# Kernel tuning notes

Measured on AMD Instinct MI355X. Metric: run time of the kernel, lower is better.

Reference implementation:

```python
import jax, jax.numpy as jnp
import numpy as np

DIM = 1024
NUM_ATT = 8
NUM_HEADS = 16
HEAD_DIM = DIM // NUM_HEADS
ROPE_BASE = 10000.0
NEG_INF = -1e9


def _rope(x):
    # x: [B, H, L, hd]; torchtune-style interleaved RoPE applied along the sequence axis.
    B, H, L, hd = x.shape
    pos = jnp.arange(L, dtype=jnp.float32)
    inv_freq = 1.0 / (ROPE_BASE ** (jnp.arange(0, hd, 2, dtype=jnp.float32) / hd))
    ang = pos[:, None] * inv_freq[None, :]          # [L, hd/2]
    cos = jnp.cos(ang)[None, None]                  # [1,1,L,hd/2]
    sin = jnp.sin(ang)[None, None]
    xr = x.reshape(B, H, L, hd // 2, 2)
    x0, x1 = xr[..., 0], xr[..., 1]
    out = jnp.stack([x0 * cos - x1 * sin, x1 * cos + x0 * sin], axis=-1)
    return out.reshape(B, H, L, hd).astype(x.dtype)


def setup_inputs() -> dict:
    key = jax.random.key(0)
    ks = jax.random.split(key, 7)
    B, L = 32, 512
    x = jax.random.normal(ks[0], (B, L, DIM), dtype=jnp.float32)
    s = 0.02  # init scale for numerical sanity (init choice, not math)
    query_projs = jax.random.normal(ks[1], (NUM_ATT, DIM, DIM), dtype=jnp.float32) * s
    key_projs = jax.random.normal(ks[2], (NUM_ATT, DIM, DIM), dtype=jnp.float32) * s
    value_projs = jax.random.normal(ks[3], (NUM_ATT, DIM, DIM), dtype=jnp.float32) * s
    out_projs = jax.random.normal(ks[4], (NUM_ATT, DIM, DIM), dtype=jnp.float32) * s
    router_w = jax.random.normal(ks[5], (DIM, NUM_ATT), dtype=jnp.float32) * s
    router_b = jnp.zeros((NUM_ATT,), dtype=jnp.float32)
    return {"x": x, "query_projs": query_projs, "key_projs": key_projs,
            "value_projs": value_projs, "out_projs": out_projs,
            "router_w": router_w, "router_b": router_b}


def reference(x, query_projs, key_projs, value_projs, out_projs, router_w, router_b):
    B, L, D = x.shape
    H, hd = NUM_HEADS, HEAD_DIM
    scale = hd ** -0.5

    # top-1 routing on mean-pooled tokens
    logits = x.mean(axis=1) @ router_w + router_b       # [B, E]
    attn_probs = jax.nn.softmax(logits, axis=-1)
    routes = jnp.argmax(attn_probs, axis=-1)            # [B] int

    # per-batch weight gather (the memory-bound irregular access) + bmm
    qw = query_projs[routes]                             # [B, D, D]
    kw = key_projs[routes]
    vw = value_projs[routes]
    q = jnp.einsum('bld,bde->ble', x, qw)
    k = jnp.einsum('bld,bde->ble', x, kw)
    v = jnp.einsum('bld,bde->ble', x, vw)

    q = q.reshape(B, L, H, hd).transpose(0, 2, 1, 3)     # [B,H,L,hd]
    k = k.reshape(B, L, H, hd).transpose(0, 2, 1, 3)
    v = v.reshape(B, L, H, hd).transpose(0, 2, 1, 3)

    q = _rope(q)
    k = _rope(k)

    scores = jnp.einsum('bhld,bhmd->bhlm', q, k) * scale  # [B,H,L,L]
    causal = jnp.triu(jnp.ones((L, L), dtype=bool), k=1)  # True above diag = masked
    scores = jnp.where(causal[None, None], NEG_INF, scores)
    attn = jax.nn.softmax(scores, axis=-1)
    out = jnp.einsum('bhlm,bhmd->bhld', attn, v)          # [B,H,L,hd]
    out = out.transpose(0, 2, 1, 3).reshape(B, L, D)

    ow = out_projs[routes]                                # [B, D, D]
    out = jnp.einsum('bld,bde->ble', out, ow)
    return out, attn_probs
```

## Files before the change

kernel.cpp:

```cpp
#include <hip/hip_runtime.h>


typedef __attribute__((ext_vector_type(8))) short bf16x8;
typedef __attribute__((ext_vector_type(4))) float f32x4;

typedef const __attribute__((address_space(1))) unsigned short* gas_t;
typedef __attribute__((address_space(3))) unsigned short* las_t;

#define OFF_PART   (0ull)
#define OFF_ROUTES (2ull << 20)
#define OFF_XB     (3ull << 20)
#define OFF_WT     (40ull << 20)
#define OFF_QKV    (112ull << 20)

__device__ __forceinline__ unsigned short f2bf(float f){
  unsigned int u = __float_as_uint(f);
  u += 0x7fffu + ((u >> 16) & 1u);
  return (unsigned short)(u >> 16);
}


__global__ void meanpool_kernel(const float* __restrict__ x, float* __restrict__ part,
                                unsigned short* __restrict__ xb){
  const int b = blockIdx.x, lc = blockIdx.y, t = threadIdx.x;
  const size_t base = ((size_t)b*512 + lc*32)*1024;
  const float* xs = x + base;
  unsigned short* xo = xb + base;
  float a0=0.f, a1=0.f, a2=0.f, a3=0.f;
  for (int l = 0; l < 32; ++l){
    const float* row = xs + l*1024;
    unsigned short* orow = xo + l*1024;
    const float v0 = row[t], v1 = row[t+256], v2 = row[t+512], v3 = row[t+768];
    a0 += v0; a1 += v1; a2 += v2; a3 += v3;
    orow[t] = f2bf(v0); orow[t+256] = f2bf(v1); orow[t+512] = f2bf(v2); orow[t+768] = f2bf(v3);
  }
  float* o = part + ((size_t)b*16 + lc)*1024;
  o[t] = a0; o[t+256] = a1; o[t+512] = a2; o[t+768] = a3;
}

__global__ void router_kernel(const float* __restrict__ part,
                              const float* __restrict__ rw,
                              const float* __restrict__ rbias,
                              float* __restrict__ probs,
                              int* __restrict__ routes){
  const int b = blockIdx.x, t = threadIdx.x;
  __shared__ float xbar[1024];
  __shared__ float red[256*8];
  #pragma unroll
  for (int k = 0; k < 4; ++k){
    const int d = t + k*256;
    float s = 0.f;
    for (int lc = 0; lc < 16; ++lc) s += part[((size_t)b*16 + lc)*1024 + d];
    xbar[d] = s * (1.0f/512.0f);
  }
  __syncthreads();
  float p[8] = {0.f,0.f,0.f,0.f,0.f,0.f,0.f,0.f};
  #pragma unroll
  for (int k = 0; k < 4; ++k){
    const int d = t + k*256;
    const float xv = xbar[d];
    #pragma unroll
    for (int e = 0; e < 8; ++e) p[e] = fmaf(xv, rw[d*8 + e], p[e]);
  }
  #pragma unroll
  for (int e = 0; e < 8; ++e) red[t*8 + e] = p[e];
  __syncthreads();
  for (int s2 = 128; s2 > 0; s2 >>= 1){
    if (t < s2){
      #pragma unroll
      for (int e = 0; e < 8; ++e) red[t*8 + e] += red[(t + s2)*8 + e];
    }
    __syncthreads();
  }
  if (t == 0){
    float lg[8], mx = -3e38f; int am = 0;
    #pragma unroll
    for (int e = 0; e < 8; ++e){
      lg[e] = red[e] + rbias[e];
      if (lg[e] > mx){ mx = lg[e]; am = e; }
    }
    float sum = 0.f, ex[8];
    #pragma unroll
    for (int e = 0; e < 8; ++e){ ex[e] = __expf(lg[e] - mx); sum += ex[e]; }
    const float inv = 1.0f / sum;
    #pragma unroll
    for (int e = 0; e < 8; ++e) probs[b*8 + e] = ex[e] * inv;
    routes[b] = am;
  }
}


__global__ void wcast_kernel(const float* __restrict__ W, unsigned short* __restrict__ Wt){
  __shared__ float tile[32][33];
  const int mtx = blockIdx.z;
  const float* Wm = W + (size_t)mtx*1024*1024;
  unsigned short* Wo = Wt + (size_t)mtx*1024*1024;
  const int t = threadIdx.x;
  const int c = t & 31, r0 = t >> 5;
  const int gx = blockIdx.x*32, gy = blockIdx.y*32;
  #pragma unroll
  for (int k = 0; k < 4; ++k){
    const int r = r0 + k*8;
    tile[r][c] = Wm[(size_t)(gy + r)*1024 + gx + c];
  }
  __syncthreads();
  #pragma unroll
  for (int k = 0; k < 4; ++k){
    const int r = r0 + k*8;
    Wo[(size_t)(gx + r)*1024 + gy + c] = f2bf(tile[c][r]);
  }
}


template<int MODE>
__global__ __launch_bounds__(256, 2) void gemm_kernel(
    const unsigned short* __restrict__ A,
    const unsigned short* __restrict__ Wt,
    const int* __restrict__ routes,
    unsigned short* __restrict__ qkvout,
    float* __restrict__ outf)
{
  __shared__ __align__(16) unsigned short As[3][128*32];
  __shared__ __align__(16) unsigned short Bs[3][128*32];

  int wg = blockIdx.x + (blockIdx.y << 3) + (blockIdx.z << 5);
  wg = (wg & 7) * ((MODE == 0) ? 384 : 128) + (wg >> 3);
  const int z   = wg >> 5;
  const int rem = wg & 31;
  const int m0  = (rem >> 3) * 128;
  const int n0  = (rem & 7) * 128;
  const int b = (MODE == 0) ? (z / 3) : z;
  const int p = (MODE == 0) ? (z - b*3) : 0;

  const int route = routes[b];
  const unsigned short* Ab = A + (size_t)b*512*1024;
  const unsigned short* Wb = Wt + (size_t)((MODE == 0) ? (p*8 + route) : route)*1024*1024;
  const int t = threadIdx.x;
  const int lane = t & 63;
  const int wave = t >> 6;
  const int wm = (wave >> 1) * 64;
  const int wn = (wave & 1) * 64;
  const int quad = lane >> 4;
  const int ln = lane & 15;

  f32x4 acc[4][4] = {};

  const int u0 = t, u1 = t + 256;
  const int r0s = u0 >> 2, c0s = (u0 & 3) ^ ((r0s >> 1) & 3);
  const int r1s = u1 >> 2, c1s = (u1 & 3) ^ ((r1s >> 1) & 3);
  const unsigned short* gA0 = Ab + (size_t)(m0 + r0s)*1024 + c0s*8;
  const unsigned short* gA1 = Ab + (size_t)(m0 + r1s)*1024 + c1s*8;
  const unsigned short* gB0 = Wb + (size_t)(n0 + r0s)*1024 + c0s*8;
  const unsigned short* gB1 = Wb + (size_t)(n0 + r1s)*1024 + c1s*8;
  las_t lA0 = (las_t)(&As[0][0] + u0*8), lA1 = (las_t)(&As[0][0] + u1*8);
  las_t lB0 = (las_t)(&Bs[0][0] + u0*8), lB1 = (las_t)(&Bs[0][0] + u1*8);

  const int swz = (quad ^ ((ln >> 1) & 3)) * 8;
  int offA[4], offB[4];
  #pragma unroll
  for (int i = 0; i < 4; ++i){
    offA[i] = (wm + i*16 + ln)*32 + swz;
    offB[i] = (wn + i*16 + ln)*32 + swz;
  }

#define STAGE(buf, kk) do { \
    const int bo_ = (buf)*4096; \
    __builtin_amdgcn_global_load_lds((gas_t)(gA0 + (kk)), lA0 + bo_, 16, 0, 0); \
    __builtin_amdgcn_global_load_lds((gas_t)(gA1 + (kk)), lA1 + bo_, 16, 0, 0); \
    __builtin_amdgcn_global_load_lds((gas_t)(gB0 + (kk)), lB0 + bo_, 16, 0, 0); \
    __builtin_amdgcn_global_load_lds((gas_t)(gB1 + (kk)), lB1 + bo_, 16, 0, 0); \
  } while (0)

#define COMPUTE(buf) do { \
    const unsigned short* Al_ = &As[buf][0]; \
    const unsigned short* Bl_ = &Bs[buf][0]; \
    bf16x8 av[4], bv[4]; \
    _Pragma("unroll") \
    for (int i = 0; i < 4; ++i){ \
      av[i] = *(const bf16x8*)(Al_ + offA[i]); \
      bv[i] = *(const bf16x8*)(Bl_ + offB[i]); \
    } \
    __builtin_amdgcn_s_setprio(1); \
    _Pragma("unroll") \
    for (int i = 0; i < 4; ++i) \
      _Pragma("unroll") \
      for (int j = 0; j < 4; ++j) \
        acc[i][j] = __builtin_amdgcn_mfma_f32_16x16x32_bf16(av[i], bv[j], acc[i][j], 0, 0, 0); \
    __builtin_amdgcn_s_setprio(0); \
  } while (0)

  STAGE(0, 0);
  STAGE(1, 32);
  for (int t8 = 0; t8 < 30; ++t8){
    asm volatile("s_waitcnt vmcnt(4)" ::: "memory");
    __builtin_amdgcn_s_barrier();
    __builtin_amdgcn_sched_barrier(0);
    STAGE((t8 + 2) % 3, t8*32 + 64);
    COMPUTE(t8 % 3);
  }
  asm volatile("s_waitcnt vmcnt(4)" ::: "memory");
  __builtin_amdgcn_s_barrier();
  __builtin_amdgcn_sched_barrier(0);
  COMPUTE(0);
  asm volatile("s_waitcnt vmcnt(0)" ::: "memory");
  __builtin_amdgcn_s_barrier();
  __builtin_amdgcn_sched_barrier(0);
  COMPUTE(1);
#undef STAGE
#undef COMPUTE

  if (MODE == 0){
    const size_t PSZ = (size_t)32*16*512*64;
    if (p < 2){
      #pragma unroll
      for (int j = 0; j < 4; ++j){
        const int e  = n0 + wn + j*16 + ln;
        const int h  = e >> 6;
        const int eh = e & 63;
        const float invf = exp2f(-0.41524101f * (float)(eh >> 1));
        float s1, c1; __sincosf(invf, &s1, &c1);
        unsigned short* outp = qkvout + ((((size_t)p*32 + b)*16 + h)*512)*64 + eh;
        const int l0 = m0 + wm + quad*4;
        #pragma unroll
        for (int i = 0; i < 4; ++i){
          float sn, cs;
          __sincosf((float)(l0 + i*16) * invf, &sn, &cs);
          #pragma unroll
          for (int r = 0; r < 4; ++r){
            const int l = l0 + i*16 + r;
            const float own = acc[i][j][r];
            const float par = __shfl_xor(own, 1, 64);
            const float v = (e & 1) ? fmaf(own, cs, par*sn) : fmaf(own, cs, -par*sn);
            outp[(size_t)l*64] = f2bf(v);
            const float nc = cs*c1 - sn*s1;
            const float ns = sn*c1 + cs*s1;
            cs = nc; sn = ns;
          }
        }
      }
    } else {
      #pragma unroll
      for (int j = 0; j < 4; ++j){
        const int e  = n0 + wn + j*16 + ln;
        const int h  = e >> 6;
        const int eh = e & 63;
        unsigned short* outp = qkvout + 2*PSZ + (((size_t)b*16 + h)*64 + eh)*512;
        #pragma unroll
        for (int i = 0; i < 4; ++i){
          const int l0 = m0 + wm + i*16 + quad*4;
          ushort4 pk;
          pk.x = f2bf(acc[i][j][0]); pk.y = f2bf(acc[i][j][1]);
          pk.z = f2bf(acc[i][j][2]); pk.w = f2bf(acc[i][j][3]);
          *(ushort4*)(outp + l0) = pk;
        }
      }
    }
  } else {
    #pragma unroll
    for (int j = 0; j < 4; ++j){
      const int e = n0 + wn + j*16 + ln;
      #pragma unroll
      for (int i = 0; i < 4; ++i){
        #pragma unroll
        for (int r = 0; r < 4; ++r){
          const int l = m0 + wm + i*16 + quad*4 + r;
          outf[((size_t)b*512 + l)*1024 + e] = acc[i][j][r];
        }
      }
    }
  }
}


#define PSTR 72

__global__ __launch_bounds__(256, 3) void attn_kernel(
    const unsigned short* __restrict__ qkv,
    unsigned short* __restrict__ ctx)
{
  __shared__ __align__(16) unsigned short Ks[2][64*64];
  __shared__ __align__(16) unsigned short Vts[2][64*64];
  __shared__ __align__(16) unsigned short Ps[4][32*PSTR];

  int wg = blockIdx.x + (blockIdx.y << 2) + (blockIdx.z << 6);
  wg = (wg & 7) * 256 + (wg >> 3);
  const int b  = wg >> 6;
  const int h  = (wg >> 2) & 15;
  const int qt = wg & 3;

  const size_t HO  = (((size_t)b)*16 + h)*512*64;
  const size_t PSZ = (size_t)32*16*512*64;
  const unsigned short* Qg  = qkv + HO;
  const unsigned short* Kg  = qkv + PSZ + HO;
  const unsigned short* Vtg = qkv + 2*PSZ + HO;

  const int t    = threadIdx.x;
  const int lane = t & 63;
  const int wave = t >> 6;
  const int quad = lane >> 4;
  const int ln   = lane & 15;

  const int u0 = t, u1 = t + 256;
  const int kr0 = u0 >> 3, kc0 = (u0 & 7) ^ (kr0 & 7);
  const int kr1 = u1 >> 3, kc1 = (u1 & 7) ^ (kr1 & 7);

  bf16x8 aq[2][2];
  #pragma unroll
  for (int rg = 0; rg < 2; ++rg){
    const int row = qt*128 + rg*64 + wave*16 + ln;
    #pragma unroll
    for (int ks = 0; ks < 2; ++ks)
      aq[rg][ks] = *(const bf16x8*)(Qg + (size_t)row*64 + ks*32 + quad*8);
  }

  const int ktEnd = 2*qt + 1;

  __builtin_amdgcn_global_load_lds((gas_t)(Kg  + kr0*64  + kc0*8), (las_t)(Ks[0]  + u0*8), 16,0,0);
  __builtin_amdgcn_global_load_lds((gas_t)(Kg  + kr1*64  + kc1*8), (las_t)(Ks[0]  + u1*8), 16,0,0);
  __builtin_amdgcn_global_load_lds((gas_t)(Vtg + kr0*512 + kc0*8), (las_t)(Vts[0] + u0*8), 16,0,0);
  __builtin_amdgcn_global_load_lds((gas_t)(Vtg + kr1*512 + kc1*8), (las_t)(Vts[0] + u1*8), 16,0,0);

  float m_r[2][4], l_r[2][4];
  #pragma unroll
  for (int rg = 0; rg < 2; ++rg)
    #pragma unroll
    for (int r = 0; r < 4; ++r){ m_r[rg][r] = -3e38f; l_r[rg][r] = 0.f; }
  f32x4 o[2][4] = {};

  const int swzl = ln & 7;
  unsigned short* Pw = Ps[wave];
  const int rowoff = wave*16 + quad*4;

  for (int kt = 0; kt <= ktEnd; ++kt){
    __syncthreads();
    if (kt < ktEnd){
      const unsigned short* Kn  = Kg + (kt+1)*4096;
      const int col = (kt+1)*64;
      unsigned short* kb = Ks[(kt+1)&1];
      unsigned short* vb = Vts[(kt+1)&1];
      __builtin_amdgcn_global_load_lds((gas_t)(Kn  + kr0*64 + kc0*8),        (las_t)(kb + u0*8), 16,0,0);
      __builtin_amdgcn_global_load_lds((gas_t)(Kn  + kr1*64 + kc1*8),        (las_t)(kb + u1*8), 16,0,0);
      __builtin_amdgcn_global_load_lds((gas_t)(Vtg + kr0*512 + col + kc0*8), (las_t)(vb + u0*8), 16,0,0);
      __builtin_amdgcn_global_load_lds((gas_t)(Vtg + kr1*512 + col + kc1*8), (las_t)(vb + u1*8), 16,0,0);
    }
    const unsigned short* ks_ = Ks[kt&1];
    const unsigned short* vt_ = Vts[kt&1];

    #pragma unroll
    for (int rg = 0; rg < 2; ++rg){
      if (rg == 0 && kt > 2*qt) continue;
      const bool diag = (kt == 2*qt + rg);

      f32x4 s[4] = {};
      __builtin_amdgcn_s_setprio(1);
      #pragma unroll
      for (int ks2 = 0; ks2 < 2; ++ks2){
        #pragma unroll
        for (int kn = 0; kn < 4; ++kn){
          const bf16x8 bk = *(const bf16x8*)(ks_ + (kn*16+ln)*64 + (((quad + ks2*4) ^ swzl))*8);
          s[kn] = __builtin_amdgcn_mfma_f32_16x16x32_bf16(aq[rg][ks2], bk, s[kn], 0, 0, 0);
        }
      }
      __builtin_amdgcn_s_setprio(0);

      float p[4][4], lm[4] = {-3e38f,-3e38f,-3e38f,-3e38f};
      #pragma unroll
      for (int kn = 0; kn < 4; ++kn){
        const int col = kn*16 + ln;
        #pragma unroll
        for (int r = 0; r < 4; ++r){
          float v = s[kn][r] * 0.125f;
          if (diag && col > rowoff + r) v = -1e9f;
          p[kn][r] = v;
          lm[r] = fmaxf(lm[r], v);
        }
      }
      #pragma unroll
      for (int off = 1; off < 16; off <<= 1)
        #pragma unroll
        for (int r = 0; r < 4; ++r)
          lm[r] = fmaxf(lm[r], __shfl_xor(lm[r], off, 64));
      float alpha[4], rsum[4];
      #pragma unroll
      for (int r = 0; r < 4; ++r){
        const float mn = fmaxf(m_r[rg][r], lm[r]);
        alpha[r] = __expf(m_r[rg][r] - mn);
        m_r[rg][r] = mn;
      }
      #pragma unroll
      for (int kn = 0; kn < 4; ++kn)
        #pragma unroll
        for (int r = 0; r < 4; ++r)
          p[kn][r] = __expf(p[kn][r] - m_r[rg][r]);
      #pragma unroll
      for (int r = 0; r < 4; ++r)
        rsum[r] = (p[0][r] + p[1][r]) + (p[2][r] + p[3][r]);
      #pragma unroll
      for (int off = 1; off < 16; off <<= 1)
        #pragma unroll
        for (int r = 0; r < 4; ++r)
          rsum[r] += __shfl_xor(rsum[r], off, 64);
      #pragma unroll
      for (int r = 0; r < 4; ++r) l_r[rg][r] = l_r[rg][r]*alpha[r] + rsum[r];
      #pragma unroll
      for (int dn = 0; dn < 4; ++dn)
        #pragma unroll
        for (int r = 0; r < 4; ++r)
          o[rg][dn][r] *= alpha[r];

      #pragma unroll
      for (int kn = 0; kn < 4; ++kn)
        #pragma unroll
        for (int r = 0; r < 4; ++r)
          Pw[(rg*16 + quad*4 + r)*PSTR + kn*16 + ln] = f2bf(p[kn][r]);

      __builtin_amdgcn_s_setprio(1);
      #pragma unroll
      for (int ks2 = 0; ks2 < 2; ++ks2){
        const bf16x8 ap = *(const bf16x8*)(Pw + (rg*16 + ln)*PSTR + quad*8 + ks2*32);
        #pragma unroll
        for (int dn = 0; dn < 4; ++dn){
          const bf16x8 bv = *(const bf16x8*)(vt_ + (dn*16+ln)*64 + (((quad + ks2*4) ^ swzl))*8);
          o[rg][dn] = __builtin_amdgcn_mfma_f32_16x16x32_bf16(ap, bv, o[rg][dn], 0, 0, 0);
        }
      }
      __builtin_amdgcn_s_setprio(0);
    }
  }

  #pragma unroll
  for (int rg = 0; rg < 2; ++rg){
    #pragma unroll
    for (int r = 0; r < 4; ++r){
      const float inv = 1.0f / l_r[rg][r];
      const int row = qt*128 + rg*64 + wave*16 + quad*4 + r;
      unsigned short* op = ctx + ((size_t)b*512 + row)*1024 + h*64 + ln;
      #pragma unroll
      for (int dn = 0; dn < 4; ++dn)
        op[dn*16] = f2bf(o[rg][dn][r] * inv);
    }
  }
}


extern "C" void kernel_launch(void* const* d_in, const int* in_sizes, int n_in,
                              void* d_out, int out_size, void* d_ws, size_t ws_size,
                              hipStream_t stream) {
  const float* x     = (const float*)d_in[0];
  const float* qw    = (const float*)d_in[1];
  const float* kw    = (const float*)d_in[2];
  const float* vw    = (const float*)d_in[3];
  const float* ow    = (const float*)d_in[4];
  const float* rw    = (const float*)d_in[5];
  const float* rbias = (const float*)d_in[6];
  float* out = (float*)d_out;
  char* ws = (char*)d_ws;

  float* part            = (float*)(ws + OFF_PART);
  int* routes            = (int*)(ws + OFF_ROUTES);
  unsigned short* xb     = (unsigned short*)(ws + OFF_XB);
  unsigned short* wt     = (unsigned short*)(ws + OFF_WT);
  unsigned short* qkvbuf = (unsigned short*)(ws + OFF_QKV);
  unsigned short* ctx    = xb;
  float* probs = out + (size_t)32*512*1024;

  meanpool_kernel<<<dim3(32, 16), 256, 0, stream>>>(x, part, xb);
  router_kernel<<<32, 256, 0, stream>>>(part, rw, rbias, probs, routes);
  wcast_kernel<<<dim3(32, 32, 8), 256, 0, stream>>>(qw, wt);
  wcast_kernel<<<dim3(32, 32, 8), 256, 0, stream>>>(kw, wt + (size_t)8*1024*1024);
  wcast_kernel<<<dim3(32, 32, 8), 256, 0, stream>>>(vw, wt + (size_t)16*1024*1024);
  wcast_kernel<<<dim3(32, 32, 8), 256, 0, stream>>>(ow, wt + (size_t)24*1024*1024);
  gemm_kernel<0><<<dim3(8, 4, 96), 256, 0, stream>>>(xb, wt, routes, qkvbuf, nullptr);
  attn_kernel<<<dim3(4, 16, 32), 256, 0, stream>>>(qkvbuf, ctx);
  gemm_kernel<1><<<dim3(8, 4, 32), 256, 0, stream>>>(ctx, wt + (size_t)24*1024*1024, routes,
                                                     nullptr, out);
}
```

Measured before the change: 523.9 us.

## Enlarge GEMM tiles to 256x256 with 8 waves and interleaved LDS-read/MFMA schedule

Rewrites the GEMM kernel to use 256x256 output tiles with K-step 64, 512 threads (8 waves each computing 128x64), and double-buffered LDS with an XOR swizzle. The main loop is split into four MFMA quadrants, with LDS fragment reads and global-to-LDS staging interleaved between barriers so memory traffic overlaps compute. The goal is more data reuse per loaded byte and better latency hiding. In exchange it needs far more LDS (128KB) and more registers, which may limit occupancy, and it makes fewer, larger workgroups.

```diff
diff --git a/kernel.cpp b/kernel.cpp
--- a/kernel.cpp
+++ b/kernel.cpp
@@ -113,122 +113,165 @@
 
 
 template<int MODE>
-__global__ __launch_bounds__(256, 2) void gemm_kernel(
+__global__ __launch_bounds__(512, 2) void gemm_kernel(
     const unsigned short* __restrict__ A,
     const unsigned short* __restrict__ Wt,
     const int* __restrict__ routes,
     unsigned short* __restrict__ qkvout,
     float* __restrict__ outf)
 {
-  __shared__ __align__(16) unsigned short As[3][128*32];
-  __shared__ __align__(16) unsigned short Bs[3][128*32];
-
-  int wg = blockIdx.x + (blockIdx.y << 3) + (blockIdx.z << 5);
-  wg = (wg & 7) * ((MODE == 0) ? 384 : 128) + (wg >> 3);
-  const int z   = wg >> 5;
-  const int rem = wg & 31;
-  const int m0  = (rem >> 3) * 128;
-  const int n0  = (rem & 7) * 128;
-  const int b = (MODE == 0) ? (z / 3) : z;
-  const int p = (MODE == 0) ? (z - b*3) : 0;
+  __shared__ __align__(16) unsigned short As[2][256*64];
+  __shared__ __align__(16) unsigned short Bs[2][256*64];
+
+  const int f = blockIdx.x + blockIdx.y*8;
+  const int CH = (MODE == 0) ? 96 : 32;
+  const int wg = (f & 7)*CH + (f >> 3);
+  const int slice = wg >> 3;
+  const int tile  = wg & 7;
+  const int m0 = (tile >> 2)*256;
+  const int n0 = (tile & 3)*256;
+  const int b = (MODE == 0) ? (slice/3) : slice;
+  const int p = (MODE == 0) ? (slice - b*3) : 0;
 
   const int route = routes[b];
   const unsigned short* Ab = A + (size_t)b*512*1024;
   const unsigned short* Wb = Wt + (size_t)((MODE == 0) ? (p*8 + route) : route)*1024*1024;
+
   const int t = threadIdx.x;
   const int lane = t & 63;
   const int wave = t >> 6;
-  const int wm = (wave >> 1) * 64;
-  const int wn = (wave & 1) * 64;
+  const int wm = (wave >> 2)*128;
+  const int wn = (wave & 3)*64;
   const int quad = lane >> 4;
   const int ln = lane & 15;
 
-  f32x4 acc[4][4] = {};
-
-  const int u0 = t, u1 = t + 256;
-  const int r0s = u0 >> 2, c0s = (u0 & 3) ^ ((r0s >> 1) & 3);
-  const int r1s = u1 >> 2, c1s = (u1 & 3) ^ ((r1s >> 1) & 3);
-  const unsigned short* gA0 = Ab + (size_t)(m0 + r0s)*1024 + c0s*8;
-  const unsigned short* gA1 = Ab + (size_t)(m0 + r1s)*1024 + c1s*8;
-  const unsigned short* gB0 = Wb + (size_t)(n0 + r0s)*1024 + c0s*8;
-  const unsigned short* gB1 = Wb + (size_t)(n0 + r1s)*1024 + c1s*8;
-  las_t lA0 = (las_t)(&As[0][0] + u0*8), lA1 = (las_t)(&As[0][0] + u1*8);
-  las_t lB0 = (las_t)(&Bs[0][0] + u0*8), lB1 = (las_t)(&Bs[0][0] + u1*8);
-
-  const int swz = (quad ^ ((ln >> 1) & 3)) * 8;
-  int offA[4], offB[4];
-  #pragma unroll
-  for (int i = 0; i < 4; ++i){
-    offA[i] = (wm + i*16 + ln)*32 + swz;
-    offB[i] = (wn + i*16 + ln)*32 + swz;
-  }
-
-#define STAGE(buf, kk) do { \
-    const int bo_ = (buf)*4096; \
-    __builtin_amdgcn_global_load_lds((gas_t)(gA0 + (kk)), lA0 + bo_, 16, 0, 0); \
-    __builtin_amdgcn_global_load_lds((gas_t)(gA1 + (kk)), lA1 + bo_, 16, 0, 0); \
-    __builtin_amdgcn_global_load_lds((gas_t)(gB0 + (kk)), lB0 + bo_, 16, 0, 0); \
-    __builtin_amdgcn_global_load_lds((gas_t)(gB1 + (kk)), lB1 + bo_, 16, 0, 0); \
+  const int srow = t >> 3;
+  const int sch  = (t & 7) ^ (srow & 7);
+  const unsigned short* gA0 = Ab + (size_t)(m0 + srow)*1024 + sch*8;
+  const unsigned short* gB0 = Wb + (size_t)(n0 + srow)*1024 + sch*8;
+
+  const int w8 = ln & 7;
+  const int aO0 = (wm + ln)*64 + ((quad    ) ^ w8)*8;
+  const int aO1 = (wm + ln)*64 + ((quad + 4) ^ w8)*8;
+  const int bO0 = (wn + ln)*64 + ((quad    ) ^ w8)*8;
+  const int bO1 = (wn + ln)*64 + ((quad + 4) ^ w8)*8;
+
+  f32x4 acc[8][4] = {};
+  bf16x8 a0[4][2], a1[4][2], b01[2][2], b23[2][2];
+
+#define STAGE(c_, T_) do { \
+    const size_t ko_ = (size_t)(T_)*64; \
+    las_t dA_ = (las_t)(&As[c_][0]) + (size_t)t*8; \
+    las_t dB_ = (las_t)(&Bs[c_][0]) + (size_t)t*8; \
+    _Pragma("unroll") \
+    for (int k_ = 0; k_ < 4; ++k_){ \
+      __builtin_amdgcn_global_load_lds((gas_t)(gA0 + ko_ + (size_t)k_*65536), dA_ + k_*4096, 16, 0, 0); \
+      __builtin_amdgcn_global_load_lds((gas_t)(gB0 + ko_ + (size_t)k_*65536), dB_ + k_*4096, 16, 0, 0); \
+    } \
   } while (0)
 
-#define COMPUTE(buf) do { \
-    const unsigned short* Al_ = &As[buf][0]; \
-    const unsigned short* Bl_ = &Bs[buf][0]; \
-    bf16x8 av[4], bv[4]; \
-    _Pragma("unroll") \
-    for (int i = 0; i < 4; ++i){ \
-      av[i] = *(const bf16x8*)(Al_ + offA[i]); \
-      bv[i] = *(const bf16x8*)(Bl_ + offB[i]); \
-    } \
-    __builtin_amdgcn_s_setprio(1); \
-    _Pragma("unroll") \
-    for (int i = 0; i < 4; ++i) \
-      _Pragma("unroll") \
-      for (int j = 0; j < 4; ++j) \
-        acc[i][j] = __builtin_amdgcn_mfma_f32_16x16x32_bf16(av[i], bv[j], acc[i][j], 0, 0, 0); \
-    __builtin_amdgcn_s_setprio(0); \
+#define RD(ptr_, off_) (*(const bf16x8*)((ptr_) + (off_)))
+#define READ_F0(pA_, pB_) do { \
+    _Pragma("unroll") for (int f_ = 0; f_ < 4; ++f_){ \
+      a0[f_][0] = RD(pA_, aO0 + f_*1024); a0[f_][1] = RD(pA_, aO1 + f_*1024); } \
+    _Pragma("unroll") for (int f_ = 0; f_ < 2; ++f_){ \
+      b01[f_][0] = RD(pB_, bO0 + f_*1024); b01[f_][1] = RD(pB_, bO1 + f_*1024); } \
   } while (0)
+#define READ_F1(pA_) do { \
+    _Pragma("unroll") for (int f_ = 0; f_ < 4; ++f_){ \
+      a1[f_][0] = RD(pA_, aO0 + (4+f_)*1024); a1[f_][1] = RD(pA_, aO1 + (4+f_)*1024); } \
+  } while (0)
+#define READ_F2(pB_) do { \
+    _Pragma("unroll") for (int f_ = 0; f_ < 2; ++f_){ \
+      b23[f_][0] = RD(pB_, bO0 + (2+f_)*1024); b23[f_][1] = RD(pB_, bO1 + (2+f_)*1024); } \
+  } while (0)
+
+#define MSET(AF_, BF_, IB_, JB_) do { \
+    _Pragma("unroll") for (int f_ = 0; f_ < 4; ++f_) \
+    _Pragma("unroll") for (int n_ = 0; n_ < 2; ++n_) \
+    _Pragma("unroll") for (int k_ = 0; k_ < 2; ++k_) \
+      acc[IB_+f_][JB_+n_] = __builtin_amdgcn_mfma_f32_16x16x32_bf16( \
+          AF_[f_][k_], BF_[n_][k_], acc[IB_+f_][JB_+n_], 0, 0, 0); \
+  } while (0)
 
   STAGE(0, 0);
-  STAGE(1, 32);
-  for (int t8 = 0; t8 < 30; ++t8){
-    asm volatile("s_waitcnt vmcnt(4)" ::: "memory");
-    __builtin_amdgcn_s_barrier();
+  STAGE(1, 1);
+  asm volatile("s_waitcnt vmcnt(8)" ::: "memory");
+  __builtin_amdgcn_s_barrier();
+  READ_F0((&As[0][0]), (&Bs[0][0]));
+
+  for (int g = 0; g < 16; ++g){
+    const int c = g & 1;
+    const unsigned short* pA  = &As[c][0];
+    const unsigned short* pB  = &Bs[c][0];
+    const unsigned short* pAn = &As[c ^ 1][0];
+    const unsigned short* pBn = &Bs[c ^ 1][0];
+
+    READ_F1(pA);
+    __builtin_amdgcn_s_barrier();
+    asm volatile("s_waitcnt lgkmcnt(8)" ::: "memory");
     __builtin_amdgcn_sched_barrier(0);
-    STAGE((t8 + 2) % 3, t8*32 + 64);
-    COMPUTE(t8 % 3);
-  }
-  asm volatile("s_waitcnt vmcnt(4)" ::: "memory");
-  __builtin_amdgcn_s_barrier();
-  __builtin_amdgcn_sched_barrier(0);
-  COMPUTE(0);
-  asm volatile("s_waitcnt vmcnt(0)" ::: "memory");
-  __builtin_amdgcn_s_barrier();
-  __builtin_amdgcn_sched_barrier(0);
-  COMPUTE(1);
+    __builtin_amdgcn_s_setprio(1);
+    MSET(a0, b01, 0, 0);
+    __builtin_amdgcn_s_setprio(0);
+    __builtin_amdgcn_s_barrier();
+
+    READ_F2(pB);
+    __builtin_amdgcn_s_barrier();
+    asm volatile("s_waitcnt lgkmcnt(4)" ::: "memory");
+    __builtin_amdgcn_sched_barrier(0);
+    __builtin_amdgcn_s_setprio(1);
+    MSET(a1, b01, 4, 0);
+    __builtin_amdgcn_s_setprio(0);
+    __builtin_amdgcn_s_barrier();
+
+    asm volatile("s_waitcnt lgkmcnt(0)" ::: "memory");
+    __builtin_amdgcn_sched_barrier(0);
+    __builtin_amdgcn_s_setprio(1);
+    MSET(a1, b23, 4, 2);
+    __builtin_amdgcn_s_setprio(0);
+    __builtin_amdgcn_s_barrier();
+
+    if (g < 14){
+      STAGE(c, g + 2);
+      asm volatile("s_waitcnt vmcnt(8)" ::: "memory");
+    } else if (g == 14){
+      asm volatile("s_waitcnt vmcnt(0)" ::: "memory");
+    }
+    __builtin_amdgcn_s_barrier();
+    __builtin_amdgcn_s_setprio(1);
+    MSET(a0, b23, 0, 2);
+    __builtin_amdgcn_s_setprio(0);
+    if (g < 15) READ_F0(pAn, pBn);
+    __builtin_amdgcn_s_barrier();
+  }
 #undef STAGE
-#undef COMPUTE
+#undef RD
+#undef READ_F0
+#undef READ_F1
+#undef READ_F2
+#undef MSET
 
   if (MODE == 0){
     const size_t PSZ = (size_t)32*16*512*64;
     if (p < 2){
       #pragma unroll
-      for (int j = 0; j < 4; ++j){
-        const int e  = n0 + wn + j*16 + ln;
+      for (int fn = 0; fn < 4; ++fn){
+        const int e  = n0 + wn + fn*16 + ln;
         const int h  = e >> 6;
         const int eh = e & 63;
         const float invf = exp2f(-0.41524101f * (float)(eh >> 1));
         float s1, c1; __sincosf(invf, &s1, &c1);
         unsigned short* outp = qkvout + ((((size_t)p*32 + b)*16 + h)*512)*64 + eh;
-        const int l0 = m0 + wm + quad*4;
-        #pragma unroll
-        for (int i = 0; i < 4; ++i){
+        #pragma unroll
+        for (int fm = 0; fm < 8; ++fm){
+          const int l0 = m0 + wm + fm*16 + quad*4;
           float sn, cs;
-          __sincosf((float)(l0 + i*16) * invf, &sn, &cs);
+          __sincosf((float)l0 * invf, &sn, &cs);
           #pragma unroll
           for (int r = 0; r < 4; ++r){
-            const int l = l0 + i*16 + r;
-            const float own = acc[i][j][r];
+            const int l = l0 + r;
+            const float own = acc[fm][fn][r];
             const float par = __shfl_xor(own, 1, 64);
             const float v = (e & 1) ? fmaf(own, cs, par*sn) : fmaf(own, cs, -par*sn);
             outp[(size_t)l*64] = f2bf(v);
@@ -240,31 +283,31 @@
       }
     } else {
       #pragma unroll
-      for (int j = 0; j < 4; ++j){
-        const int e  = n0 + wn + j*16 + ln;
+      for (int fn = 0; fn < 4; ++fn){
+        const int e  = n0 + wn + fn*16 + ln;
         const int h  = e >> 6;
         const int eh = e & 63;
         unsigned short* outp = qkvout + 2*PSZ + (((size_t)b*16 + h)*64 + eh)*512;
         #pragma unroll
-        for (int i = 0; i < 4; ++i){
-          const int l0 = m0 + wm + i*16 + quad*4;
+        for (int fm = 0; fm < 8; ++fm){
+          const int l0 = m0 + wm + fm*16 + quad*4;
           ushort4 pk;
-          pk.x = f2bf(acc[i][j][0]); pk.y = f2bf(acc[i][j][1]);
-          pk.z = f2bf(acc[i][j][2]); pk.w = f2bf(acc[i][j][3]);
+          pk.x = f2bf(acc[fm][fn][0]); pk.y = f2bf(acc[fm][fn][1]);
+          pk.z = f2bf(acc[fm][fn][2]); pk.w = f2bf(acc[fm][fn][3]);
           *(ushort4*)(outp + l0) = pk;
         }
       }
     }
   } else {
     #pragma unroll
-    for (int j = 0; j < 4; ++j){
-      const int e = n0 + wn + j*16 + ln;
-      #pragma unroll
-      for (int i = 0; i < 4; ++i){
+    for (int fn = 0; fn < 4; ++fn){
+      const int e = n0 + wn + fn*16 + ln;
+      #pragma unroll
+      for (int fm = 0; fm < 8; ++fm){
         #pragma unroll
         for (int r = 0; r < 4; ++r){
-          const int l = m0 + wm + i*16 + quad*4 + r;
-          outf[((size_t)b*512 + l)*1024 + e] = acc[i][j][r];
+          const int l = m0 + wm + fm*16 + quad*4 + r;
+          outf[((size_t)b*512 + l)*1024 + e] = acc[fm][fn][r];
         }
       }
     }
@@ -470,8 +513,8 @@
   wcast_kernel<<<dim3(32, 32, 8), 256, 0, stream>>>(kw, wt + (size_t)8*1024*1024);
   wcast_kernel<<<dim3(32, 32, 8), 256, 0, stream>>>(vw, wt + (size_t)16*1024*1024);
   wcast_kernel<<<dim3(32, 32, 8), 256, 0, stream>>>(ow, wt + (size_t)24*1024*1024);
-  gemm_kernel<0><<<dim3(8, 4, 96), 256, 0, stream>>>(xb, wt, routes, qkvbuf, nullptr);
+  gemm_kernel<0><<<dim3(8, 96), 512, 0, stream>>>(xb, wt, routes, qkvbuf, nullptr);
   attn_kernel<<<dim3(4, 16, 32), 256, 0, stream>>>(qkvbuf, ctx);
-  gemm_kernel<1><<<dim3(8, 4, 32), 256, 0, stream>>>(ctx, wt + (size_t)24*1024*1024, routes,
-                                                     nullptr, out);
-}
+  gemm_kernel<1><<<dim3(8, 32), 512, 0, stream>>>(ctx, wt + (size_t)24*1024*1024, routes,
+                                                  nullptr, out);
+}
```

Result: no change. 516.2 us (-1.5%).
